# Optimization experiments

Measured on AMD Instinct MI355X. Metric: run time of the kernel, lower is better.

## Reference

```python
import jax, jax.numpy as jnp
import numpy as np

N, T, D, H = 8, 1024, 128, 8

def setup_inputs() -> dict:
    key = jax.random.key(0)
    ks = jax.random.split(key, 6)
    x = jax.random.normal(ks[0], (N, T, D), dtype=jnp.float32)
    attention_mask = jax.random.randint(ks[1], (N, 1, 1, T), 0, 2).astype(jnp.bool_)
    attention_weights = jax.random.uniform(ks[2], (N, H, T, T), dtype=jnp.float32)
    # Linear(dim -> heads*dim) weights, torch convention: W @ x^T + b, W: [H*D, D]
    s = 1.0 / np.sqrt(D)
    Wq = jax.random.normal(ks[3], (H * D, D), dtype=jnp.float32) * s
    Wk = jax.random.normal(ks[4], (H * D, D), dtype=jnp.float32) * s
    Wv = jax.random.normal(ks[5], (H * D, D), dtype=jnp.float32) * s
    bq = jnp.zeros((H * D,), jnp.float32)
    bk = jnp.zeros((H * D,), jnp.float32)
    bv = jnp.zeros((H * D,), jnp.float32)
    return {"x": x, "attention_mask": attention_mask, "attention_weights": attention_weights,
            "Wq": Wq, "bq": bq, "Wk": Wk, "bk": bk, "Wv": Wv, "bv": bv}

def reference(x, attention_mask, attention_weights, Wq, bq, Wk, bk, Wv, bv):
    n, t, d = x.shape
    h = Wq.shape[0] // d
    # projections: [N,T,H*D] -> [N,H,T,D]
    q = (x @ Wq.T + bq).reshape(n, t, h, d).transpose(0, 2, 1, 3)
    k = (x @ Wk.T + bk).reshape(n, t, h, d).transpose(0, 2, 1, 3)
    v = (x @ Wv.T + bv).reshape(n, t, h, d).transpose(0, 2, 1, 3)
    # scores [N,H,T,T]
    att = jnp.einsum('nhtd,nhsd->nhts', q, k) / np.sqrt(d).astype(np.float32)
    att = att * attention_weights
    att = jnp.where(attention_mask, -jnp.inf, att)
    att = jax.nn.softmax(att, axis=-1)
    out = jnp.einsum('nhts,nhsd->nhtd', att, v)
    out = out.transpose(0, 2, 1, 3).reshape(n, t, h * d)
    out_agg = jnp.mean(out, axis=1)
    return out, jax.lax.stop_gradient(out_agg), jax.lax.stop_gradient(att)
```

## Files before the change

### kernel.cpp

```cpp
#include <hip/hip_runtime.h>
#include <hip/hip_bf16.h>
#include <hip/hip_fp16.h>

#define NB 8
#define TT 1024
#define DD 128
#define HH 8

using short8  = __attribute__((ext_vector_type(8))) short;
using floatx4 = __attribute__((ext_vector_type(4))) float;
using half8   = __attribute__((ext_vector_type(8))) _Float16;

__device__ __forceinline__ unsigned short f2bf_u(float f) {
    union { float f; unsigned u; } v; v.f = f;
    return (unsigned short)((v.u + 0x7fffu + ((v.u >> 16) & 1u)) >> 16);
}

__global__ __launch_bounds__(256, 2) void proj_kernel(
    const float* __restrict__ x,
    const float* __restrict__ Wq, const float* __restrict__ bq,
    const float* __restrict__ Wk, const float* __restrict__ bk,
    const float* __restrict__ Wv, const float* __restrict__ bv,
    unsigned short* __restrict__ qb, unsigned short* __restrict__ kb,
    unsigned short* __restrict__ vt)
{
    int b     = blockIdx.x;
    int which = b >> 10;
    int rem   = b & 1023;
    int mblk  = rem >> 3;
    int nblk  = rem & 7;
    int tid   = threadIdx.x;
    int wid   = tid >> 6, lane = tid & 63;
    int l15   = lane & 15, quad = lane >> 4;
    int m0    = mblk * 64 + wid * 16;

    const float* W    = (which == 0) ? Wq : (which == 1) ? Wk : Wv;
    const float* bias = (which == 0) ? bq : (which == 1) ? bk : bv;
    unsigned short* dst = (which == 0) ? qb : (which == 1) ? kb : vt;

    short8 a[4];
    const float* xr = x + (size_t)(m0 + l15) * DD + quad * 8;
    #pragma unroll
    for (int kk = 0; kk < 4; ++kk) {
        const float* p = xr + kk * 32;
        short8 t;
        #pragma unroll
        for (int j = 0; j < 8; ++j) t[j] = (short)f2bf_u(p[j]);
        a[kk] = t;
    }

    floatx4 acc[8];
    #pragma unroll
    for (int ct = 0; ct < 8; ++ct) acc[ct] = (floatx4){0.f, 0.f, 0.f, 0.f};

    for (int ct = 0; ct < 8; ++ct) {
        int c = nblk * 128 + ct * 16 + l15;
        const float* wr = W + (size_t)c * DD + quad * 8;
        #pragma unroll
        for (int kk = 0; kk < 4; ++kk) {
            const float* p = wr + kk * 32;
            short8 bf;
            #pragma unroll
            for (int j = 0; j < 8; ++j) bf[j] = (short)f2bf_u(p[j]);
            acc[ct] = __builtin_amdgcn_mfma_f32_16x16x32_bf16(a[kk], bf, acc[ct], 0, 0, 0);
        }
    }

    #pragma unroll
    for (int ct = 0; ct < 8; ++ct) {
        int c  = nblk * 128 + ct * 16 + l15;
        int h  = c >> 7, dd = c & 127;
        float bsv = bias[c];
        #pragma unroll
        for (int r = 0; r < 4; ++r) {
            int m = m0 + quad * 4 + r;
            int n = m >> 10, t = m & 1023;
            unsigned short v = f2bf_u(acc[ct][r] + bsv);
            size_t idx;
            if (which == 2) idx = ((size_t)(n * HH + h) * DD + dd) * TT + t;
            else            idx = ((size_t)(n * HH + h) * TT + t) * DD + dd;
            dst[idx] = v;
        }
    }
}

#define SSTRIDE 1032

__global__ __launch_bounds__(256, 2) void attn_kernel(
    const unsigned short* __restrict__ qb, const unsigned short* __restrict__ kb,
    const unsigned short* __restrict__ vt,
    const float* __restrict__ wts, const int* __restrict__ mask,
    float* __restrict__ out, float* __restrict__ outagg, float* __restrict__ att)
{
    extern __shared__ char smem[];
    _Float16* S   = (_Float16*)smem;
    float* rowinv = (float*)(smem + 32 * SSTRIDE * 2);

    int b    = blockIdx.x;
    int slot = b & 7, j = b >> 3;
    int tile = j & 31, gq = j >> 5;
    int g    = gq * 8 + slot;
    int n    = g >> 3, h = g & 7;
    int t0   = tile * 32;

    int tid = threadIdx.x;
    int wid = tid >> 6, lane = tid & 63;
    int l15 = lane & 15, quad = lane >> 4;

    const unsigned short* qp = qb + ((size_t)g * TT + t0) * DD;
    const unsigned short* kp = kb + (size_t)g * TT * DD;
    const unsigned short* vp = vt + (size_t)g * DD * TT;
    const float* wp = wts + (size_t)g * TT * TT + (size_t)t0 * TT;
    const int*   mp = mask + n * TT;
    float* attp = att + (size_t)g * TT * TT + (size_t)t0 * TT;

    short8 aq[2][4];
    #pragma unroll
    for (int rt = 0; rt < 2; ++rt)
        #pragma unroll
        for (int kk = 0; kk < 4; ++kk)
            aq[rt][kk] = *(const short8*)(qp + (size_t)(rt * 16 + l15) * DD + kk * 32 + quad * 8);

    const int c0 = wid * 256;
    const float scale = 0.08838834764831845f;
    for (int ct = 0; ct < 16; ++ct) {
        int scol = c0 + ct * 16;
        int mk = mp[scol + l15];
        float w0[4], w1[4];
        #pragma unroll
        for (int r = 0; r < 4; ++r) {
            int row = quad * 4 + r;
            w0[r] = wp[(size_t)row * TT + scol + l15];
            w1[r] = wp[(size_t)(row + 16) * TT + scol + l15];
        }
        floatx4 acc0 = {0.f,0.f,0.f,0.f}, acc1 = {0.f,0.f,0.f,0.f};
        #pragma unroll
        for (int kk = 0; kk < 4; ++kk) {
            short8 bf = *(const short8*)(kp + (size_t)(scol + l15) * DD + kk * 32 + quad * 8);
            acc0 = __builtin_amdgcn_mfma_f32_16x16x32_bf16(aq[0][kk], bf, acc0, 0, 0, 0);
            acc1 = __builtin_amdgcn_mfma_f32_16x16x32_bf16(aq[1][kk], bf, acc1, 0, 0, 0);
        }
        #pragma unroll
        for (int r = 0; r < 4; ++r) {
            int row = quad * 4 + r;
            float s0 = mk ? -65504.f : acc0[r] * scale * w0[r];
            float s1 = mk ? -65504.f : acc1[r] * scale * w1[r];
            S[row * SSTRIDE + scol + l15]        = (_Float16)s0;
            S[(row + 16) * SSTRIDE + scol + l15] = (_Float16)s1;
        }
    }
    __syncthreads();

    int row = tid >> 3;
    int jj  = tid & 7;
    _Float16* Srow = S + row * SSTRIDE + jj * 8;

    float mx = -3.0e38f;
    #pragma unroll 4
    for (int i = 0; i < 16; ++i) {
        half8 hv = *(const half8*)(Srow + i * 64);
        #pragma unroll
        for (int e = 0; e < 8; ++e) mx = fmaxf(mx, (float)hv[e]);
    }
    mx = fmaxf(mx, __shfl_xor(mx, 1));
    mx = fmaxf(mx, __shfl_xor(mx, 2));
    mx = fmaxf(mx, __shfl_xor(mx, 4));

    float sum = 0.f;
    #pragma unroll 4
    for (int i = 0; i < 16; ++i) {
        half8 hv = *(const half8*)(Srow + i * 64);
        #pragma unroll
        for (int e = 0; e < 8; ++e) sum += __expf((float)hv[e] - mx);
    }
    sum += __shfl_xor(sum, 1);
    sum += __shfl_xor(sum, 2);
    sum += __shfl_xor(sum, 4);
    float iv = 1.f / sum;
    if (jj == 0) rowinv[row] = iv;

    float* arow = attp + (size_t)row * TT + jj * 8;
    #pragma unroll 2
    for (int i = 0; i < 16; ++i) {
        half8 hv = *(const half8*)(Srow + i * 64);
        half8 ev;
        floatx4 o0, o1;
        #pragma unroll
        for (int e = 0; e < 8; ++e) {
            float ex = __expf((float)hv[e] - mx);
            ev[e] = __builtin_bit_cast(_Float16, f2bf_u(ex));
            float a = ex * iv;
            if (e < 4) o0[e] = a; else o1[e - 4] = a;
        }
        *(half8*)(Srow + i * 64) = ev;
        *(floatx4*)(arow + i * 64)     = o0;
        *(floatx4*)(arow + i * 64 + 4) = o1;
    }
    __syncthreads();

    int c0p = wid * 32;
    floatx4 o00 = {0.f,0.f,0.f,0.f}, o01 = o00, o10 = o00, o11 = o00;
    #pragma unroll 2
    for (int ks = 0; ks < 32; ++ks) {
        short8 a0 = __builtin_bit_cast(short8,
            *(const half8*)(S + (size_t)l15 * SSTRIDE + ks * 32 + quad * 8));
        short8 a1 = __builtin_bit_cast(short8,
            *(const half8*)(S + (size_t)(16 + l15) * SSTRIDE + ks * 32 + quad * 8));
        short8 b0 = *(const short8*)(vp + (size_t)(c0p + l15) * TT + ks * 32 + quad * 8);
        short8 b1 = *(const short8*)(vp + (size_t)(c0p + 16 + l15) * TT + ks * 32 + quad * 8);
        o00 = __builtin_amdgcn_mfma_f32_16x16x32_bf16(a0, b0, o00, 0, 0, 0);
        o01 = __builtin_amdgcn_mfma_f32_16x16x32_bf16(a0, b1, o01, 0, 0, 0);
        o10 = __builtin_amdgcn_mfma_f32_16x16x32_bf16(a1, b0, o10, 0, 0, 0);
        o11 = __builtin_amdgcn_mfma_f32_16x16x32_bf16(a1, b1, o11, 0, 0, 0);
    }

    #pragma unroll
    for (int ct = 0; ct < 2; ++ct) {
        int col = c0p + ct * 16 + l15;
        float agg = 0.f;
        #pragma unroll
        for (int rt = 0; rt < 2; ++rt) {
            floatx4 oo = (rt == 0) ? (ct == 0 ? o00 : o01) : (ct == 0 ? o10 : o11);
            #pragma unroll
            for (int r = 0; r < 4; ++r) {
                int rw = rt * 16 + quad * 4 + r;
                float val = oo[r] * rowinv[rw];
                out[((size_t)(n * TT + t0 + rw)) * (HH * DD) + h * DD + col] = val;
                agg += val;
            }
        }
        atomicAdd(outagg + n * (HH * DD) + h * DD + col, agg * (1.f / (float)TT));
    }
}

extern "C" void kernel_launch(void* const* d_in, const int* in_sizes, int n_in,
                              void* d_out, int out_size, void* d_ws, size_t ws_size,
                              hipStream_t stream) {
    const float* x    = (const float*)d_in[0];
    const int*   mask = (const int*)d_in[1];
    const float* wts  = (const float*)d_in[2];
    const float* Wq = (const float*)d_in[3];
    const float* bq = (const float*)d_in[4];
    const float* Wk = (const float*)d_in[5];
    const float* bk = (const float*)d_in[6];
    const float* Wv = (const float*)d_in[7];
    const float* bv = (const float*)d_in[8];

    float* out    = (float*)d_out;
    float* outagg = out + (size_t)NB * TT * HH * DD;
    float* att    = outagg + NB * HH * DD;

    unsigned short* qb = (unsigned short*)d_ws;
    unsigned short* kb = qb + (size_t)NB * HH * TT * DD;
    unsigned short* vt = kb + (size_t)NB * HH * TT * DD;

    hipMemsetAsync(outagg, 0, (size_t)NB * HH * DD * sizeof(float), stream);
    proj_kernel<<<3072, 256, 0, stream>>>(x, Wq, bq, Wk, bk, Wv, bv, qb, kb, vt);
    attn_kernel<<<2048, 256, 32 * SSTRIDE * 2 + 128, stream>>>(
        qb, kb, vt, wts, mask, out, outagg, att);
}
```

Baseline: 773.5 us.

## Pre-convert projection weights to bf16 and halve attention query tile to 16 rows

Adds a small kernel that converts Wq/Wk/Wv to bf16 once per call, so the projection kernel loads packed bf16 vectors instead of converting fp32 weights per element. The attention kernel now processes 16 query rows per block instead of 32, which halves shared memory per block and doubles the grid, and launch bounds are raised to target higher occupancy. The cost is that each K and V tile is reused across half as many query rows, so K/V global traffic doubles, and there is one extra kernel launch.

```diff
diff --git a/kernel.cpp b/kernel.cpp
--- a/kernel.cpp
+++ b/kernel.cpp
@@ -16,11 +16,27 @@
     return (unsigned short)((v.u + 0x7fffu + ((v.u >> 16) & 1u)) >> 16);
 }
 
-__global__ __launch_bounds__(256, 2) void proj_kernel(
-    const float* __restrict__ x,
-    const float* __restrict__ Wq, const float* __restrict__ bq,
-    const float* __restrict__ Wk, const float* __restrict__ bk,
-    const float* __restrict__ Wv, const float* __restrict__ bv,
+__global__ __launch_bounds__(256) void convw_kernel(
+    const float* __restrict__ Wq, const float* __restrict__ Wk,
+    const float* __restrict__ Wv, unsigned short* __restrict__ Wb)
+{
+    int idx = blockIdx.x * 256 + threadIdx.x;
+    const int NW = HH * DD * DD / 4;
+    const float* src; unsigned short* dst; int off = idx;
+    if (idx < NW)          { src = Wq; dst = Wb; }
+    else if (idx < 2 * NW) { src = Wk; dst = Wb + HH * DD * DD;     off = idx - NW; }
+    else                   { src = Wv; dst = Wb + 2 * HH * DD * DD; off = idx - 2 * NW; }
+    float4 v = ((const float4*)src)[off];
+    union { unsigned short u[4]; uint2 w; } o;
+    o.u[0] = f2bf_u(v.x); o.u[1] = f2bf_u(v.y);
+    o.u[2] = f2bf_u(v.z); o.u[3] = f2bf_u(v.w);
+    *(uint2*)(dst + (size_t)off * 4) = o.w;
+}
+
+__global__ __launch_bounds__(256, 4) void proj_kernel(
+    const float* __restrict__ x, const unsigned short* __restrict__ Wb,
+    const float* __restrict__ bq, const float* __restrict__ bk,
+    const float* __restrict__ bv,
     unsigned short* __restrict__ qb, unsigned short* __restrict__ kb,
     unsigned short* __restrict__ vt)
 {
@@ -34,7 +50,7 @@
     int l15   = lane & 15, quad = lane >> 4;
     int m0    = mblk * 64 + wid * 16;
 
-    const float* W    = (which == 0) ? Wq : (which == 1) ? Wk : Wv;
+    const unsigned short* W = Wb + (size_t)which * HH * DD * DD;
     const float* bias = (which == 0) ? bq : (which == 1) ? bk : bv;
     unsigned short* dst = (which == 0) ? qb : (which == 1) ? kb : vt;
 
@@ -55,13 +71,10 @@
 
     for (int ct = 0; ct < 8; ++ct) {
         int c = nblk * 128 + ct * 16 + l15;
-        const float* wr = W + (size_t)c * DD + quad * 8;
+        const unsigned short* wr = W + (size_t)c * DD + quad * 8;
         #pragma unroll
         for (int kk = 0; kk < 4; ++kk) {
-            const float* p = wr + kk * 32;
-            short8 bf;
-            #pragma unroll
-            for (int j = 0; j < 8; ++j) bf[j] = (short)f2bf_u(p[j]);
+            short8 bf = *(const short8*)(wr + kk * 32);
             acc[ct] = __builtin_amdgcn_mfma_f32_16x16x32_bf16(a[kk], bf, acc[ct], 0, 0, 0);
         }
     }
@@ -86,7 +99,7 @@
 
 #define SSTRIDE 1032
 
-__global__ __launch_bounds__(256, 2) void attn_kernel(
+__global__ __launch_bounds__(256, 4) void attn_kernel(
     const unsigned short* __restrict__ qb, const unsigned short* __restrict__ kb,
     const unsigned short* __restrict__ vt,
     const float* __restrict__ wts, const int* __restrict__ mask,
@@ -94,14 +107,14 @@
 {
     extern __shared__ char smem[];
     _Float16* S   = (_Float16*)smem;
-    float* rowinv = (float*)(smem + 32 * SSTRIDE * 2);
+    float* rowinv = (float*)(smem + 16 * SSTRIDE * 2);
 
     int b    = blockIdx.x;
     int slot = b & 7, j = b >> 3;
-    int tile = j & 31, gq = j >> 5;
+    int tile = j & 63, gq = j >> 6;
     int g    = gq * 8 + slot;
     int n    = g >> 3, h = g & 7;
-    int t0   = tile * 32;
+    int t0   = tile * 16;
 
     int tid = threadIdx.x;
     int wid = tid >> 6, lane = tid & 63;
@@ -114,75 +127,69 @@
     const int*   mp = mask + n * TT;
     float* attp = att + (size_t)g * TT * TT + (size_t)t0 * TT;
 
-    short8 aq[2][4];
-    #pragma unroll
-    for (int rt = 0; rt < 2; ++rt)
-        #pragma unroll
-        for (int kk = 0; kk < 4; ++kk)
-            aq[rt][kk] = *(const short8*)(qp + (size_t)(rt * 16 + l15) * DD + kk * 32 + quad * 8);
+    short8 aq[4];
+    #pragma unroll
+    for (int kk = 0; kk < 4; ++kk)
+        aq[kk] = *(const short8*)(qp + (size_t)l15 * DD + kk * 32 + quad * 8);
 
     const int c0 = wid * 256;
     const float scale = 0.08838834764831845f;
     for (int ct = 0; ct < 16; ++ct) {
         int scol = c0 + ct * 16;
         int mk = mp[scol + l15];
-        float w0[4], w1[4];
+        float w0[4];
+        #pragma unroll
+        for (int r = 0; r < 4; ++r)
+            w0[r] = wp[(size_t)(quad * 4 + r) * TT + scol + l15];
+        floatx4 acc = {0.f, 0.f, 0.f, 0.f};
+        #pragma unroll
+        for (int kk = 0; kk < 4; ++kk) {
+            short8 bf = *(const short8*)(kp + (size_t)(scol + l15) * DD + kk * 32 + quad * 8);
+            acc = __builtin_amdgcn_mfma_f32_16x16x32_bf16(aq[kk], bf, acc, 0, 0, 0);
+        }
         #pragma unroll
         for (int r = 0; r < 4; ++r) {
             int row = quad * 4 + r;
-            w0[r] = wp[(size_t)row * TT + scol + l15];
-            w1[r] = wp[(size_t)(row + 16) * TT + scol + l15];
-        }
-        floatx4 acc0 = {0.f,0.f,0.f,0.f}, acc1 = {0.f,0.f,0.f,0.f};
-        #pragma unroll
-        for (int kk = 0; kk < 4; ++kk) {
-            short8 bf = *(const short8*)(kp + (size_t)(scol + l15) * DD + kk * 32 + quad * 8);
-            acc0 = __builtin_amdgcn_mfma_f32_16x16x32_bf16(aq[0][kk], bf, acc0, 0, 0, 0);
-            acc1 = __builtin_amdgcn_mfma_f32_16x16x32_bf16(aq[1][kk], bf, acc1, 0, 0, 0);
-        }
-        #pragma unroll
-        for (int r = 0; r < 4; ++r) {
-            int row = quad * 4 + r;
-            float s0 = mk ? -65504.f : acc0[r] * scale * w0[r];
-            float s1 = mk ? -65504.f : acc1[r] * scale * w1[r];
-            S[row * SSTRIDE + scol + l15]        = (_Float16)s0;
-            S[(row + 16) * SSTRIDE + scol + l15] = (_Float16)s1;
+            float s = mk ? -65504.f : acc[r] * scale * w0[r];
+            S[row * SSTRIDE + scol + l15] = (_Float16)s;
         }
     }
     __syncthreads();
 
-    int row = tid >> 3;
-    int jj  = tid & 7;
+    int row = tid >> 4;
+    int jj  = tid & 15;
     _Float16* Srow = S + row * SSTRIDE + jj * 8;
 
     float mx = -3.0e38f;
-    #pragma unroll 4
-    for (int i = 0; i < 16; ++i) {
-        half8 hv = *(const half8*)(Srow + i * 64);
+    #pragma unroll
+    for (int i = 0; i < 8; ++i) {
+        half8 hv = *(const half8*)(Srow + i * 128);
         #pragma unroll
         for (int e = 0; e < 8; ++e) mx = fmaxf(mx, (float)hv[e]);
     }
     mx = fmaxf(mx, __shfl_xor(mx, 1));
     mx = fmaxf(mx, __shfl_xor(mx, 2));
     mx = fmaxf(mx, __shfl_xor(mx, 4));
+    mx = fmaxf(mx, __shfl_xor(mx, 8));
 
     float sum = 0.f;
-    #pragma unroll 4
-    for (int i = 0; i < 16; ++i) {
-        half8 hv = *(const half8*)(Srow + i * 64);
+    #pragma unroll
+    for (int i = 0; i < 8; ++i) {
+        half8 hv = *(const half8*)(Srow + i * 128);
         #pragma unroll
         for (int e = 0; e < 8; ++e) sum += __expf((float)hv[e] - mx);
     }
     sum += __shfl_xor(sum, 1);
     sum += __shfl_xor(sum, 2);
     sum += __shfl_xor(sum, 4);
+    sum += __shfl_xor(sum, 8);
     float iv = 1.f / sum;
     if (jj == 0) rowinv[row] = iv;
 
     float* arow = attp + (size_t)row * TT + jj * 8;
     #pragma unroll 2
-    for (int i = 0; i < 16; ++i) {
-        half8 hv = *(const half8*)(Srow + i * 64);
+    for (int i = 0; i < 8; ++i) {
+        half8 hv = *(const half8*)(Srow + i * 128);
         half8 ev;
         floatx4 o0, o1;
         #pragma unroll
@@ -192,42 +199,35 @@
             float a = ex * iv;
             if (e < 4) o0[e] = a; else o1[e - 4] = a;
         }
-        *(half8*)(Srow + i * 64) = ev;
-        *(floatx4*)(arow + i * 64)     = o0;
-        *(floatx4*)(arow + i * 64 + 4) = o1;
+        *(half8*)(Srow + i * 128) = ev;
+        *(floatx4*)(arow + i * 128)     = o0;
+        *(floatx4*)(arow + i * 128 + 4) = o1;
     }
     __syncthreads();
 
     int c0p = wid * 32;
-    floatx4 o00 = {0.f,0.f,0.f,0.f}, o01 = o00, o10 = o00, o11 = o00;
+    floatx4 o00 = {0.f,0.f,0.f,0.f}, o01 = o00;
     #pragma unroll 2
     for (int ks = 0; ks < 32; ++ks) {
         short8 a0 = __builtin_bit_cast(short8,
             *(const half8*)(S + (size_t)l15 * SSTRIDE + ks * 32 + quad * 8));
-        short8 a1 = __builtin_bit_cast(short8,
-            *(const half8*)(S + (size_t)(16 + l15) * SSTRIDE + ks * 32 + quad * 8));
         short8 b0 = *(const short8*)(vp + (size_t)(c0p + l15) * TT + ks * 32 + quad * 8);
         short8 b1 = *(const short8*)(vp + (size_t)(c0p + 16 + l15) * TT + ks * 32 + quad * 8);
         o00 = __builtin_amdgcn_mfma_f32_16x16x32_bf16(a0, b0, o00, 0, 0, 0);
         o01 = __builtin_amdgcn_mfma_f32_16x16x32_bf16(a0, b1, o01, 0, 0, 0);
-        o10 = __builtin_amdgcn_mfma_f32_16x16x32_bf16(a1, b0, o10, 0, 0, 0);
-        o11 = __builtin_amdgcn_mfma_f32_16x16x32_bf16(a1, b1, o11, 0, 0, 0);
     }
 
     #pragma unroll
     for (int ct = 0; ct < 2; ++ct) {
         int col = c0p + ct * 16 + l15;
+        floatx4 oo = ct ? o01 : o00;
         float agg = 0.f;
         #pragma unroll
-        for (int rt = 0; rt < 2; ++rt) {
-            floatx4 oo = (rt == 0) ? (ct == 0 ? o00 : o01) : (ct == 0 ? o10 : o11);
-            #pragma unroll
-            for (int r = 0; r < 4; ++r) {
-                int rw = rt * 16 + quad * 4 + r;
-                float val = oo[r] * rowinv[rw];
-                out[((size_t)(n * TT + t0 + rw)) * (HH * DD) + h * DD + col] = val;
-                agg += val;
-            }
+        for (int r = 0; r < 4; ++r) {
+            int rw = quad * 4 + r;
+            float val = oo[r] * rowinv[rw];
+            out[((size_t)(n * TT + t0 + rw)) * (HH * DD) + h * DD + col] = val;
+            agg += val;
         }
         atomicAdd(outagg + n * (HH * DD) + h * DD + col, agg * (1.f / (float)TT));
     }
@@ -253,9 +253,11 @@
     unsigned short* qb = (unsigned short*)d_ws;
     unsigned short* kb = qb + (size_t)NB * HH * TT * DD;
     unsigned short* vt = kb + (size_t)NB * HH * TT * DD;
+    unsigned short* Wb = vt + (size_t)NB * HH * TT * DD;
 
     hipMemsetAsync(outagg, 0, (size_t)NB * HH * DD * sizeof(float), stream);
-    proj_kernel<<<3072, 256, 0, stream>>>(x, Wq, bq, Wk, bk, Wv, bv, qb, kb, vt);
-    attn_kernel<<<2048, 256, 32 * SSTRIDE * 2 + 128, stream>>>(
+    convw_kernel<<<384, 256, 0, stream>>>(Wq, Wk, Wv, Wb);
+    proj_kernel<<<3072, 256, 0, stream>>>(x, Wb, bq, bk, bv, qb, kb, vt);
+    attn_kernel<<<4096, 256, 16 * SSTRIDE * 2 + 64, stream>>>(
         qb, kb, vt, wts, mask, out, outagg, att);
 }
```

New measurement: 800.5 us. 3.5% more time.
